# Performance work log

Hardware: AMD Instinct MI355X
Metric: run time of the kernel (lower is better)

## Reference

```python
import jax, jax.numpy as jnp
import numpy as np

N_NODES = 20000
N_EDGES = 640000
HIDDEN = 256
MSG = 64  # discrete message of MSG binary symbols -> 2*MSG one-hot bits
TAU = 0.5


def setup_inputs() -> dict:
    key = jax.random.key(0)
    ks = jax.random.split(key, 12)
    x = jax.random.normal(ks[0], (N_NODES, HIDDEN), dtype=jnp.float32)
    h = jax.random.normal(ks[1], (N_NODES, HIDDEN), dtype=jnp.float32)
    src = jax.random.randint(ks[2], (N_EDGES,), 0, N_NODES)
    dst = jax.random.randint(ks[3], (N_EDGES,), 0, N_NODES)
    u = jax.random.uniform(ks[4], (N_EDGES, MSG, 2), dtype=jnp.float32,
                           minval=1e-6, maxval=1.0 - 1e-6)
    gumbel = -jnp.log(-jnp.log(u))  # standard Gumbel noise
    def lin(k, out_f, in_f):
        bound = 1.0 / np.sqrt(in_f)
        kw, kb = jax.random.split(k)
        W = jax.random.uniform(kw, (out_f, in_f), jnp.float32, -bound, bound)
        b = jax.random.uniform(kb, (out_f,), jnp.float32, -bound, bound)
        return W, b
    W_enc, b_enc = lin(ks[5], 2 * MSG, 2 * HIDDEN)          # f_enc
    W_dec, b_dec = lin(ks[6], 2 * MSG, 2 * MSG)             # f_dec
    W_ih, b_ih = lin(ks[7], 3 * HIDDEN, HIDDEN + 2 * MSG)   # GRUCell input weights
    W_hh, b_hh = lin(ks[8], 3 * HIDDEN, HIDDEN)             # GRUCell hidden weights
    return dict(x=x, h=h, W_enc=W_enc, b_enc=b_enc, W_dec=W_dec, b_dec=b_dec,
                W_ih=W_ih, b_ih=b_ih, W_hh=W_hh, b_hh=b_hh,
                gumbel=gumbel, src=src, dst=dst)


def reference(x, h, W_enc, b_enc, W_dec, b_dec, W_ih, b_ih, W_hh, b_hh,
              gumbel, src, dst):
    N = x.shape[0]
    h_det = jax.lax.stop_gradient(h)  # edges.src['h'] uses h.detach()
    # --- msg_func: per-edge encode + straight-through gumbel-softmax (hard) ---
    e_in = jnp.concatenate([x[src], h_det[src]], axis=1)           # [E, 2H]
    logits = (e_in @ W_enc.T + b_enc).reshape(-1, MSG, 2)          # [E, M, 2]
    y_soft = jax.nn.softmax((logits + gumbel) / TAU, axis=-1)
    y_hard = jax.nn.one_hot(jnp.argmax(y_soft, axis=-1), 2, dtype=y_soft.dtype)
    m = (y_hard + y_soft - jax.lax.stop_gradient(y_soft)).reshape(-1, 2 * MSG)
    # --- aggr_func: elementwise-OR == segment max over destination nodes ---
    c = jax.ops.segment_max(m, dst, num_segments=N)
    c = jnp.where(jnp.isneginf(c), 0.0, c)  # nodes with no in-edges get zeros
    # --- update: f_dec + GRUCell (PyTorch gate order r, z, n) ---
    inp = jnp.concatenate([x, c @ W_dec.T + b_dec], axis=1)        # [N, H+2M]
    gi = inp @ W_ih.T + b_ih                                       # [N, 3H]
    gh = h @ W_hh.T + b_hh                                         # [N, 3H]
    i_r, i_z, i_n = jnp.split(gi, 3, axis=1)
    h_r, h_z, h_n = jnp.split(gh, 3, axis=1)
    r = jax.nn.sigmoid(i_r + h_r)
    z = jax.nn.sigmoid(i_z + h_z)
    n = jnp.tanh(i_n + r * h_n)
    return (1.0 - z) * n + z * h
```

## Files before the change

kernel.cpp:

```cpp
#include <hip/hip_runtime.h>
#include <math.h>

#define NN 20000
#define NE 640000

typedef __attribute__((ext_vector_type(8))) short short8v;
typedef __attribute__((ext_vector_type(4))) float f32x4;

__device__ inline unsigned short f2bf(float f) {
    unsigned int u = __builtin_bit_cast(unsigned int, f);
    u += 0x7fff + ((u >> 16) & 1);
    return (unsigned short)(u >> 16);
}
__device__ inline float bf2f(unsigned short s) {
    unsigned int u = ((unsigned int)s) << 16;
    return __builtin_bit_cast(float, u);
}
__device__ inline void gload16(const unsigned short* g, short* l) {
    __builtin_amdgcn_global_load_lds(
        (const __attribute__((address_space(1))) unsigned int*)g,
        (__attribute__((address_space(3))) unsigned int*)l, 16, 0, 0);
}

__global__ __launch_bounds__(512)
void enc_prep(const float* __restrict__ x, const float* __restrict__ h,
              const float* __restrict__ W_enc, const float* __restrict__ b_enc,
              const float* __restrict__ W_ih, const float* __restrict__ W_hh,
              const float* __restrict__ W_dec, const float* __restrict__ b_ih,
              const float* __restrict__ b_hh, const float* __restrict__ b_dec,
              unsigned short* __restrict__ LdiffBf, unsigned short* __restrict__ Abig,
              unsigned short* __restrict__ Wbig, float* __restrict__ bias_cat,
              unsigned int* __restrict__ cbits)
{
    const int tid = threadIdx.x;
    if (blockIdx.x >= 313) {
        const int r = blockIdx.x - 313;
        int zi = r * 512 + tid;
        if (zi < NN * 4) cbits[zi] = 0u;
        const int g = r >> 8, j = r & 255;
        {
            float v;
            if (tid < 256) {
                v = (g < 3) ? W_ih[(size_t)(g * 256 + j) * 384 + tid] : 0.f;
            } else {
                int sr = (g < 2) ? g * 256 + j : 512 + j;
                v = (g == 2) ? 0.f : W_hh[(size_t)sr * 256 + (tid - 256)];
            }
            Wbig[(size_t)r * 640 + tid] = f2bf(v);
        }
        if (tid < 128) {
            float acc = 0.f;
            if (g < 3) {
                const float* wr = W_ih + (size_t)(g * 256 + j) * 384 + 256;
#pragma unroll 4
                for (int p = 0; p < 128; ++p) acc += wr[p] * W_dec[p * 128 + tid];
            }
            Wbig[(size_t)r * 640 + 512 + tid] = f2bf(acc);
        } else if (tid < 192) {
            int m = tid - 128;
            float v = 0.f;
            if (g < 3) {
                const float* wr = W_ih + (size_t)(g * 256 + j) * 384 + 256;
                v = wr[m] * b_dec[m] + wr[m + 64] * b_dec[m + 64];
            }
#pragma unroll
            for (int o = 1; o < 64; o <<= 1) v += __shfl_xor(v, o);
            if (m == 0) {
                float bv;
                if (g == 3) bv = b_hh[512 + j];
                else {
                    int sr = g * 256 + j;
                    bv = b_ih[sr] + v + ((g < 2) ? b_hh[sr] : 0.f);
                }
                bias_cat[r] = bv;
            }
        }
        return;
    }
    __shared__ __align__(16) short Ah[64][72], Al[64][72];
    __shared__ __align__(16) short Wh[128 * 64], Wl[128 * 64];
    const int bm0 = blockIdx.x * 64;
    const int lane = tid & 63;
    const int wave = tid >> 6;
    const int wm = wave >> 2, wn = wave & 3;
    const int r16 = lane & 15, kg = lane >> 4;
    const int sw = r16 & 7;

    const int arow = tid >> 3, as_ = tid & 7;
    const int agm = (bm0 + arow >= NN) ? NN - 1 : bm0 + arow;
    const int wrow0 = tid >> 3, wrow1 = (tid >> 3) + 64, ws_ = tid & 7;

    f32x4 acc[2][2];
#pragma unroll
    for (int i = 0; i < 2; ++i)
#pragma unroll
        for (int j = 0; j < 2; ++j) acc[i][j] = (f32x4){0.f, 0.f, 0.f, 0.f};

    float4 av0, av1, wv0, wv1, wv2, wv3;
    auto ISSUE = [&](int kt) {
        int kc = kt * 64 + as_ * 8;
        const float* p = (kc < 256) ? (x + (size_t)agm * 256 + kc)
                                    : (h + (size_t)agm * 256 + (kc - 256));
        av0 = *(const float4*)p;
        av1 = *(const float4*)(p + 4);
        const float* q0 = W_enc + (size_t)wrow0 * 512 + kt * 64 + ws_ * 8;
        const float* q1 = W_enc + (size_t)wrow1 * 512 + kt * 64 + ws_ * 8;
        wv0 = *(const float4*)q0; wv1 = *(const float4*)(q0 + 4);
        wv2 = *(const float4*)q1; wv3 = *(const float4*)(q1 + 4);
    };

    ISSUE(0);
    for (int kt = 0; kt < 8; ++kt) {
        __syncthreads();
        {
            float vv[8] = {av0.x, av0.y, av0.z, av0.w, av1.x, av1.y, av1.z, av1.w};
            short8v hi, lo;
#pragma unroll
            for (int t = 0; t < 8; ++t) {
                unsigned short hb = f2bf(vv[t]);
                hi[t] = (short)hb;
                lo[t] = (short)f2bf(vv[t] - bf2f(hb));
            }
            *(short8v*)&Ah[arow][as_ * 8] = hi;
            *(short8v*)&Al[arow][as_ * 8] = lo;
            __builtin_nontemporal_store(
                hi, (short8v*)&Abig[(size_t)agm * 512 + kt * 64 + as_ * 8]);
            float ww0[8] = {wv0.x, wv0.y, wv0.z, wv0.w, wv1.x, wv1.y, wv1.z, wv1.w};
            float ww1[8] = {wv2.x, wv2.y, wv2.z, wv2.w, wv3.x, wv3.y, wv3.z, wv3.w};
            short8v h0, l0, h1, l1;
#pragma unroll
            for (int t = 0; t < 8; ++t) {
                unsigned short hb0 = f2bf(ww0[t]);
                h0[t] = (short)hb0; l0[t] = (short)f2bf(ww0[t] - bf2f(hb0));
                unsigned short hb1 = f2bf(ww1[t]);
                h1[t] = (short)hb1; l1[t] = (short)f2bf(ww1[t] - bf2f(hb1));
            }
            int p0 = (ws_ ^ (wrow0 & 7)) * 8;
            int p1 = (ws_ ^ (wrow1 & 7)) * 8;
            *(short8v*)&Wh[wrow0 * 64 + p0] = h0;
            *(short8v*)&Wl[wrow0 * 64 + p0] = l0;
            *(short8v*)&Wh[wrow1 * 64 + p1] = h1;
            *(short8v*)&Wl[wrow1 * 64 + p1] = l1;
        }
        if (kt < 7) ISSUE(kt + 1);
        __syncthreads();
#pragma unroll
        for (int ks = 0; ks < 2; ++ks) {
            int kc = ks * 32 + kg * 8;
            int gsel = (ks * 4 + kg) ^ sw;
            short8v ah[2], al[2], wh[2], wl[2];
#pragma unroll
            for (int f = 0; f < 2; ++f) {
                ah[f] = *(const short8v*)&Ah[wm * 32 + f * 16 + r16][kc];
                al[f] = *(const short8v*)&Al[wm * 32 + f * 16 + r16][kc];
                int wr = wn * 32 + f * 16 + r16;
                wh[f] = *(const short8v*)&Wh[wr * 64 + gsel * 8];
                wl[f] = *(const short8v*)&Wl[wr * 64 + gsel * 8];
            }
#pragma unroll
            for (int fi = 0; fi < 2; ++fi)
#pragma unroll
                for (int fj = 0; fj < 2; ++fj) {
                    acc[fi][fj] = __builtin_amdgcn_mfma_f32_16x16x32_bf16(
                        ah[fi], wh[fj], acc[fi][fj], 0, 0, 0);
                    acc[fi][fj] = __builtin_amdgcn_mfma_f32_16x16x32_bf16(
                        al[fi], wh[fj], acc[fi][fj], 0, 0, 0);
                    acc[fi][fj] = __builtin_amdgcn_mfma_f32_16x16x32_bf16(
                        ah[fi], wl[fj], acc[fi][fj], 0, 0, 0);
                }
        }
    }
#pragma unroll
    for (int fi = 0; fi < 2; ++fi) {
        int rg = bm0 + wm * 32 + fi * 16 + kg * 4;
#pragma unroll
        for (int fj = 0; fj < 2; ++fj) {
            int cg = wn * 32 + fj * 16 + r16;
            float bv = b_enc[cg];
#pragma unroll
            for (int i = 0; i < 4; ++i) {
                float v = acc[fi][fj][i] + bv;
                float o = __shfl_xor(v, 1);
                if (!(r16 & 1) && rg + i < NN)
                    LdiffBf[(size_t)(rg + i) * 64 + (cg >> 1)] = f2bf(v - o);
            }
        }
    }
}

__global__ __launch_bounds__(256)
void edge_msg_kernel(const unsigned short* __restrict__ LdiffBf,
                     const float* __restrict__ gumbel,
                     const int* __restrict__ src, const int* __restrict__ dst,
                     unsigned long long* __restrict__ cbits64, int E)
{
    const int lane = threadIdx.x & 63;
    const int hl = lane & 31;
    const int side = lane >> 5;
    const int slot = blockIdx.x * 4 + (threadIdx.x >> 6);
    const int nslots = gridDim.x * 4;
    const unsigned int* Lw = (const unsigned int*)LdiffBf;

    int p0 = slot;
    if (p0 * 2 >= E) return;
    int e0 = p0 * 2 + side;
    int s0 = src[e0], d0n = dst[e0];
    f32x4 g0 = __builtin_nontemporal_load(
        (const f32x4*)&gumbel[(size_t)e0 * 128 + hl * 4]);
    unsigned int L0 = Lw[(size_t)s0 * 32 + hl];
    int p1 = p0 + nslots;
    int s1 = 0, d1n = 0;
    if (p1 * 2 < E) { int e1 = p1 * 2 + side; s1 = src[e1]; d1n = dst[e1]; }

    while (true) {
        const bool more1 = p1 * 2 < E;
        f32x4 g1; unsigned int L1 = 0;
        if (more1) {
            int e1 = p1 * 2 + side;
            g1 = __builtin_nontemporal_load(
                (const f32x4*)&gumbel[(size_t)e1 * 128 + hl * 4]);
            L1 = Lw[(size_t)s1 * 32 + hl];
        }
        int p2 = p1 + nslots;
        int s2 = 0, d2n = 0;
        if (p2 * 2 < E) { int e2 = p2 * 2 + side; s2 = src[e2]; d2n = dst[e2]; }
        float da = bf2f((unsigned short)(L0 & 0xffffu));
        float db = bf2f((unsigned short)(L0 >> 16));
        int c0 = (da + g0[0]) < g0[1] ? 1 : 0;
        int c1 = (db + g0[2]) < g0[3] ? 1 : 0;
        int sh = (hl & 7) * 4;
        unsigned int val = (1u << (sh + c0)) | (1u << (sh + 2 + c1));
        val |= __shfl_xor(val, 1);
        val |= __shfl_xor(val, 2);
        val |= __shfl_xor(val, 4);
        unsigned int hiw = __shfl_xor(val, 8);
        if ((hl & 15) == 0)
            atomicOr(&cbits64[(size_t)d0n * 2 + (hl >> 4)],
                     (unsigned long long)val | ((unsigned long long)hiw << 32));
        if (!more1) break;
        p0 = p1; s0 = s1; d0n = d1n; g0 = g1; L0 = L1;
        p1 = p2; s1 = s2; d1n = d2n;
    }
}

__global__ __launch_bounds__(256)
void gates_gru(const unsigned short* __restrict__ Abig,
               const unsigned int* __restrict__ cbits,
               const unsigned short* __restrict__ Wbig,
               const float* __restrict__ bias_cat,
               const float* __restrict__ h, float* __restrict__ out)
{
    __shared__ __align__(16) short As[2][64 * 64];
    const int orig = blockIdx.x;
    const int xcd = orig & 7, idx = orig >> 3;
    const int wgid = (xcd < 4 ? xcd * 157 : 628 + (xcd - 4) * 156) + idx;
    const int bm0 = (wgid >> 2) * 64;
    const int j0  = (wgid & 3) * 64;
    const int tid = threadIdx.x;
    const int lane = tid & 63;
    const int w = tid >> 6;
    const int r16 = lane & 15, kg = lane >> 4;
    const int sw = r16 & 7;

    f32x4 acc[4][4];
#pragma unroll
    for (int g = 0; g < 4; ++g)
#pragma unroll
        for (int i = 0; i < 4; ++i) acc[g][i] = (f32x4){0.f, 0.f, 0.f, 0.f};

    unsigned int cw[4][4];
#pragma unroll
    for (int fi = 0; fi < 4; ++fi) {
        int rr = bm0 + fi * 16 + r16; if (rr >= NN) rr = NN - 1;
        uint4 v = *(const uint4*)&cbits[rr * 4];
        cw[fi][0] = v.x; cw[fi][1] = v.y; cw[fi][2] = v.z; cw[fi][3] = v.w;
    }

    auto STAGE = [&](int b, int kt) {
        const int kc0 = kt * 64;
#pragma unroll
        for (int it = 0; it < 2; ++it) {
            int chunk = w * 2 + it;
            int slot = chunk * 64 + lane;
            int row = slot >> 3, gch = slot & 7;
            int gm = bm0 + row; if (gm >= NN) gm = NN - 1;
            gload16(Abig + (size_t)gm * 512 + kc0 + ((gch ^ (row & 7)) << 3),
                    As[b] + chunk * 512);
        }
    };
    short8v breg[2][3][2];
    auto BLOAD = [&](int b, int kt) {
        const int kc0 = kt * 64;
        const int g2 = (kt < 4 || kt >= 8) ? 2 : 3;
#pragma unroll
        for (int s = 0; s < 3; ++s) {
            int gate = (s < 2) ? s : g2;
            const unsigned short* bp =
                Wbig + (size_t)(gate * 256 + j0 + w * 16 + r16) * 640 + kc0 + kg * 8;
            breg[b][s][0] = *(const short8v*)bp;
            breg[b][s][1] = *(const short8v*)(bp + 32);
        }
    };

    STAGE(0, 0);
    BLOAD(0, 0);
#pragma unroll
    for (int kt = 0; kt < 8; ++kt) {
        const int cur = kt & 1;
        if (kt < 7) STAGE(cur ^ 1, kt + 1);
        BLOAD(cur ^ 1, kt + 1);
        if (kt < 7) { asm volatile("s_waitcnt vmcnt(8)" ::: "memory"); }
        else        { asm volatile("s_waitcnt vmcnt(6)" ::: "memory"); }
        __builtin_amdgcn_s_barrier();
        __builtin_amdgcn_sched_barrier(0);
        const int g2c = (kt < 4) ? 2 : 3;
        __builtin_amdgcn_s_setprio(1);
#pragma unroll
        for (int ks = 0; ks < 2; ++ks) {
            int gsel = (ks * 4 + kg) ^ sw;
            short8v a[4];
#pragma unroll
            for (int fi = 0; fi < 4; ++fi)
                a[fi] = *(const short8v*)&As[cur][(fi * 16 + r16) * 64 + gsel * 8];
#pragma unroll
            for (int s = 0; s < 3; ++s) {
                const int gate = (s < 2) ? s : g2c;
#pragma unroll
                for (int fi = 0; fi < 4; ++fi)
                    acc[gate][fi] = __builtin_amdgcn_mfma_f32_16x16x32_bf16(
                        a[fi], breg[cur][s][ks], acc[gate][fi], 0, 0, 0);
            }
        }
        __builtin_amdgcn_s_setprio(0);
        __builtin_amdgcn_sched_barrier(0);
        __builtin_amdgcn_s_barrier();
    }
    BLOAD(1, 9);
#pragma unroll
    for (int kt8 = 0; kt8 < 2; ++kt8) {
        short8v a[4][2];
#pragma unroll
        for (int fi = 0; fi < 4; ++fi)
#pragma unroll
            for (int ks = 0; ks < 2; ++ks) {
                unsigned int byte = (cw[fi][kt8 * 2 + ks] >> (kg * 8)) & 0xffu;
                short8v v;
#pragma unroll
                for (int t = 0; t < 8; ++t)
                    v[t] = ((byte >> t) & 1u) ? (short)0x3F80 : (short)0;
                a[fi][ks] = v;
            }
#pragma unroll
        for (int ks = 0; ks < 2; ++ks)
#pragma unroll
            for (int s = 0; s < 3; ++s) {
                const int gate = (s < 2) ? s : 2;
#pragma unroll
                for (int fi = 0; fi < 4; ++fi)
                    acc[gate][fi] = __builtin_amdgcn_mfma_f32_16x16x32_bf16(
                        a[fi][ks], breg[kt8][s][ks], acc[gate][fi], 0, 0, 0);
            }
    }
    const int cg = j0 + w * 16 + r16;
    const float br = bias_cat[cg],       bz = bias_cat[256 + cg];
    const float bi = bias_cat[512 + cg], bh = bias_cat[768 + cg];
#pragma unroll
    for (int fi = 0; fi < 4; ++fi) {
        int rg = bm0 + fi * 16 + kg * 4;
#pragma unroll
        for (int i = 0; i < 4; ++i) {
            int m = rg + i;
            if (m >= NN) continue;
            float rp = acc[0][fi][i] + br;
            float zp = acc[1][fi][i] + bz;
            float ip = acc[2][fi][i] + bi;
            float hp = acc[3][fi][i] + bh;
            float hv = h[(size_t)m * 256 + cg];
            float r = 1.f / (1.f + __expf(-rp));
            float z = 1.f / (1.f + __expf(-zp));
            float nn2 = tanhf(ip + r * hp);
            __builtin_nontemporal_store((1.f - z) * nn2 + z * hv,
                                        &out[(size_t)m * 256 + cg]);
        }
    }
}

extern "C" void kernel_launch(void* const* d_in, const int* in_sizes, int n_in,
                              void* d_out, int out_size, void* d_ws, size_t ws_size,
                              hipStream_t stream)
{
    const float* x     = (const float*)d_in[0];
    const float* h     = (const float*)d_in[1];
    const float* W_enc = (const float*)d_in[2];
    const float* b_enc = (const float*)d_in[3];
    const float* W_dec = (const float*)d_in[4];
    const float* b_dec = (const float*)d_in[5];
    const float* W_ih  = (const float*)d_in[6];
    const float* b_ih  = (const float*)d_in[7];
    const float* W_hh  = (const float*)d_in[8];
    const float* b_hh  = (const float*)d_in[9];
    const float* gumbel = (const float*)d_in[10];
    const int*   src   = (const int*)d_in[11];
    const int*   dst   = (const int*)d_in[12];
    float* out = (float*)d_out;

    char* ws = (char*)d_ws;
    unsigned short* LdiffBf  = (unsigned short*)(ws);
    unsigned int*   cbits    = (unsigned int*)(ws + 2560000);
    unsigned short* Wbig     = (unsigned short*)(ws + 2880000);
    float*          bias_cat = (float*)(ws + 4190720);
    unsigned short* Abig     = (unsigned short*)(ws + 4194816);

    enc_prep<<<1337, 512, 0, stream>>>(x, h, W_enc, b_enc, W_ih, W_hh, W_dec,
                                       b_ih, b_hh, b_dec,
                                       LdiffBf, Abig, Wbig, bias_cat, cbits);
    edge_msg_kernel<<<4096, 256, 0, stream>>>(LdiffBf, gumbel, src, dst,
                                              (unsigned long long*)cbits, NE);
    gates_gru<<<1252, 256, 0, stream>>>(Abig, cbits, Wbig, bias_cat, h, out);
}
```

Baseline: 156.1 us.

## Overlap edge messaging with x/h gate GEMM and split c-dependent tail

Merges the edge message/atomic-OR pass and the x/h part of the GRU gate GEMM into one launch, with block index choosing the role. The goal is to let the memory-bound edge scatter run at the same time as the MFMA-heavy GEMM. Because the GEMM no longer waits for the aggregated bits, its partial accumulators go to a bf16 preactivation buffer. A new tail kernel reloads them, adds the c·W contribution from the bit-packed messages, and applies the GRU nonlinearity. The cost is an extra round trip of preactivations through global memory and bf16 rounding of those partial sums, which may reduce accuracy. It also drops the nontemporal hint on the Abig store, likely to keep the data cache-resident.

```diff
diff --git a/kernel.cpp b/kernel.cpp
--- a/kernel.cpp
+++ b/kernel.cpp
@@ -123,8 +123,7 @@
             }
             *(short8v*)&Ah[arow][as_ * 8] = hi;
             *(short8v*)&Al[arow][as_ * 8] = lo;
-            __builtin_nontemporal_store(
-                hi, (short8v*)&Abig[(size_t)agm * 512 + kt * 64 + as_ * 8]);
+            *(short8v*)&Abig[(size_t)agm * 512 + kt * 64 + as_ * 8] = hi;
             float ww0[8] = {wv0.x, wv0.y, wv0.z, wv0.w, wv1.x, wv1.y, wv1.z, wv1.w};
             float ww1[8] = {wv2.x, wv2.y, wv2.z, wv2.w, wv3.x, wv3.y, wv3.z, wv3.w};
             short8v h0, l0, h1, l1;
@@ -189,74 +188,71 @@
 }
 
 __global__ __launch_bounds__(256)
-void edge_msg_kernel(const unsigned short* __restrict__ LdiffBf,
-                     const float* __restrict__ gumbel,
-                     const int* __restrict__ src, const int* __restrict__ dst,
-                     unsigned long long* __restrict__ cbits64, int E)
+void edge_gatesxh(const unsigned short* __restrict__ LdiffBf,
+                  const float* __restrict__ gumbel,
+                  const int* __restrict__ src, const int* __restrict__ dst,
+                  unsigned long long* __restrict__ cbits64,
+                  const unsigned short* __restrict__ Abig,
+                  const unsigned short* __restrict__ Wbig,
+                  unsigned short* __restrict__ preact, int E)
 {
-    const int lane = threadIdx.x & 63;
-    const int hl = lane & 31;
-    const int side = lane >> 5;
-    const int slot = blockIdx.x * 4 + (threadIdx.x >> 6);
-    const int nslots = gridDim.x * 4;
-    const unsigned int* Lw = (const unsigned int*)LdiffBf;
-
-    int p0 = slot;
-    if (p0 * 2 >= E) return;
-    int e0 = p0 * 2 + side;
-    int s0 = src[e0], d0n = dst[e0];
-    f32x4 g0 = __builtin_nontemporal_load(
-        (const f32x4*)&gumbel[(size_t)e0 * 128 + hl * 4]);
-    unsigned int L0 = Lw[(size_t)s0 * 32 + hl];
-    int p1 = p0 + nslots;
-    int s1 = 0, d1n = 0;
-    if (p1 * 2 < E) { int e1 = p1 * 2 + side; s1 = src[e1]; d1n = dst[e1]; }
-
-    while (true) {
-        const bool more1 = p1 * 2 < E;
-        f32x4 g1; unsigned int L1 = 0;
-        if (more1) {
-            int e1 = p1 * 2 + side;
-            g1 = __builtin_nontemporal_load(
-                (const f32x4*)&gumbel[(size_t)e1 * 128 + hl * 4]);
-            L1 = Lw[(size_t)s1 * 32 + hl];
-        }
-        int p2 = p1 + nslots;
-        int s2 = 0, d2n = 0;
-        if (p2 * 2 < E) { int e2 = p2 * 2 + side; s2 = src[e2]; d2n = dst[e2]; }
-        float da = bf2f((unsigned short)(L0 & 0xffffu));
-        float db = bf2f((unsigned short)(L0 >> 16));
-        int c0 = (da + g0[0]) < g0[1] ? 1 : 0;
-        int c1 = (db + g0[2]) < g0[3] ? 1 : 0;
-        int sh = (hl & 7) * 4;
-        unsigned int val = (1u << (sh + c0)) | (1u << (sh + 2 + c1));
-        val |= __shfl_xor(val, 1);
-        val |= __shfl_xor(val, 2);
-        val |= __shfl_xor(val, 4);
-        unsigned int hiw = __shfl_xor(val, 8);
-        if ((hl & 15) == 0)
-            atomicOr(&cbits64[(size_t)d0n * 2 + (hl >> 4)],
-                     (unsigned long long)val | ((unsigned long long)hiw << 32));
-        if (!more1) break;
-        p0 = p1; s0 = s1; d0n = d1n; g0 = g1; L0 = L1;
-        p1 = p2; s1 = s2; d1n = d2n;
-    }
-}
-
-__global__ __launch_bounds__(256)
-void gates_gru(const unsigned short* __restrict__ Abig,
-               const unsigned int* __restrict__ cbits,
-               const unsigned short* __restrict__ Wbig,
-               const float* __restrict__ bias_cat,
-               const float* __restrict__ h, float* __restrict__ out)
-{
+    const int tid = threadIdx.x;
+    if (blockIdx.x < 2048) {
+        const int lane = tid & 63;
+        const int hl = lane & 31;
+        const int side = lane >> 5;
+        const int slot = blockIdx.x * 4 + (tid >> 6);
+        const int nslots = 2048 * 4;
+        const unsigned int* Lw = (const unsigned int*)LdiffBf;
+
+        int p0 = slot;
+        if (p0 * 2 >= E) return;
+        int e0 = p0 * 2 + side;
+        int s0 = src[e0], d0n = dst[e0];
+        f32x4 g0 = __builtin_nontemporal_load(
+            (const f32x4*)&gumbel[(size_t)e0 * 128 + hl * 4]);
+        unsigned int L0 = Lw[(size_t)s0 * 32 + hl];
+        int p1 = p0 + nslots;
+        int s1 = 0, d1n = 0;
+        if (p1 * 2 < E) { int e1 = p1 * 2 + side; s1 = src[e1]; d1n = dst[e1]; }
+
+        while (true) {
+            const bool more1 = p1 * 2 < E;
+            f32x4 g1; unsigned int L1 = 0;
+            if (more1) {
+                int e1 = p1 * 2 + side;
+                g1 = __builtin_nontemporal_load(
+                    (const f32x4*)&gumbel[(size_t)e1 * 128 + hl * 4]);
+                L1 = Lw[(size_t)s1 * 32 + hl];
+            }
+            int p2 = p1 + nslots;
+            int s2 = 0, d2n = 0;
+            if (p2 * 2 < E) { int e2 = p2 * 2 + side; s2 = src[e2]; d2n = dst[e2]; }
+            float da = bf2f((unsigned short)(L0 & 0xffffu));
+            float db = bf2f((unsigned short)(L0 >> 16));
+            int c0 = (da + g0[0]) < g0[1] ? 1 : 0;
+            int c1 = (db + g0[2]) < g0[3] ? 1 : 0;
+            int sh = (hl & 7) * 4;
+            unsigned int val = (1u << (sh + c0)) | (1u << (sh + 2 + c1));
+            val |= __shfl_xor(val, 1);
+            val |= __shfl_xor(val, 2);
+            val |= __shfl_xor(val, 4);
+            unsigned int hiw = __shfl_xor(val, 8);
+            if ((hl & 15) == 0)
+                atomicOr(&cbits64[(size_t)d0n * 2 + (hl >> 4)],
+                         (unsigned long long)val | ((unsigned long long)hiw << 32));
+            if (!more1) break;
+            p0 = p1; s0 = s1; d0n = d1n; g0 = g1; L0 = L1;
+            p1 = p2; s1 = s2; d1n = d2n;
+        }
+        return;
+    }
     __shared__ __align__(16) short As[2][64 * 64];
-    const int orig = blockIdx.x;
+    const int orig = blockIdx.x - 2048;
     const int xcd = orig & 7, idx = orig >> 3;
     const int wgid = (xcd < 4 ? xcd * 157 : 628 + (xcd - 4) * 156) + idx;
     const int bm0 = (wgid >> 2) * 64;
     const int j0  = (wgid & 3) * 64;
-    const int tid = threadIdx.x;
     const int lane = tid & 63;
     const int w = tid >> 6;
     const int r16 = lane & 15, kg = lane >> 4;
@@ -267,14 +263,6 @@
     for (int g = 0; g < 4; ++g)
 #pragma unroll
         for (int i = 0; i < 4; ++i) acc[g][i] = (f32x4){0.f, 0.f, 0.f, 0.f};
-
-    unsigned int cw[4][4];
-#pragma unroll
-    for (int fi = 0; fi < 4; ++fi) {
-        int rr = bm0 + fi * 16 + r16; if (rr >= NN) rr = NN - 1;
-        uint4 v = *(const uint4*)&cbits[rr * 4];
-        cw[fi][0] = v.x; cw[fi][1] = v.y; cw[fi][2] = v.z; cw[fi][3] = v.w;
-    }
 
     auto STAGE = [&](int b, int kt) {
         const int kc0 = kt * 64;
@@ -291,7 +279,7 @@
     short8v breg[2][3][2];
     auto BLOAD = [&](int b, int kt) {
         const int kc0 = kt * 64;
-        const int g2 = (kt < 4 || kt >= 8) ? 2 : 3;
+        const int g2 = (kt < 4) ? 2 : 3;
 #pragma unroll
         for (int s = 0; s < 3; ++s) {
             int gate = (s < 2) ? s : g2;
@@ -307,10 +295,13 @@
 #pragma unroll
     for (int kt = 0; kt < 8; ++kt) {
         const int cur = kt & 1;
-        if (kt < 7) STAGE(cur ^ 1, kt + 1);
-        BLOAD(cur ^ 1, kt + 1);
-        if (kt < 7) { asm volatile("s_waitcnt vmcnt(8)" ::: "memory"); }
-        else        { asm volatile("s_waitcnt vmcnt(6)" ::: "memory"); }
+        if (kt < 7) {
+            STAGE(cur ^ 1, kt + 1);
+            BLOAD(cur ^ 1, kt + 1);
+            asm volatile("s_waitcnt vmcnt(8)" ::: "memory");
+        } else {
+            asm volatile("s_waitcnt vmcnt(0)" ::: "memory");
+        }
         __builtin_amdgcn_s_barrier();
         __builtin_amdgcn_sched_barrier(0);
         const int g2c = (kt < 4) ? 2 : 3;
@@ -335,7 +326,68 @@
         __builtin_amdgcn_sched_barrier(0);
         __builtin_amdgcn_s_barrier();
     }
-    BLOAD(1, 9);
+    const int cg = j0 + w * 16 + r16;
+#pragma unroll
+    for (int g = 0; g < 4; ++g)
+#pragma unroll
+        for (int fi = 0; fi < 4; ++fi) {
+            int rg = bm0 + fi * 16 + kg * 4;
+#pragma unroll
+            for (int i = 0; i < 4; ++i) {
+                int m = rg + i;
+                if (m < NN)
+                    __builtin_nontemporal_store(
+                        f2bf(acc[g][fi][i]),
+                        &preact[(size_t)m * 1024 + g * 256 + cg]);
+            }
+        }
+}
+
+__global__ __launch_bounds__(256)
+void gru_ctail(const unsigned short* __restrict__ preact,
+               const unsigned int* __restrict__ cbits,
+               const unsigned short* __restrict__ Wbig,
+               const float* __restrict__ bias_cat,
+               const float* __restrict__ h, float* __restrict__ out)
+{
+    const int wgid = blockIdx.x;
+    const int bm0 = (wgid >> 2) * 64;
+    const int j0  = (wgid & 3) * 64;
+    const int tid = threadIdx.x;
+    const int lane = tid & 63;
+    const int w = tid >> 6;
+    const int r16 = lane & 15, kg = lane >> 4;
+    const int cg = j0 + w * 16 + r16;
+
+    unsigned int cw[4][4];
+#pragma unroll
+    for (int fi = 0; fi < 4; ++fi) {
+        int rr = bm0 + fi * 16 + r16; if (rr >= NN) rr = NN - 1;
+        uint4 v = *(const uint4*)&cbits[rr * 4];
+        cw[fi][0] = v.x; cw[fi][1] = v.y; cw[fi][2] = v.z; cw[fi][3] = v.w;
+    }
+    short8v breg[2][3][2];
+#pragma unroll
+    for (int kt8 = 0; kt8 < 2; ++kt8)
+#pragma unroll
+        for (int s = 0; s < 3; ++s) {
+            const unsigned short* bp =
+                Wbig + (size_t)(s * 256 + j0 + w * 16 + r16) * 640 + (8 + kt8) * 64 + kg * 8;
+            breg[kt8][s][0] = *(const short8v*)bp;
+            breg[kt8][s][1] = *(const short8v*)(bp + 32);
+        }
+    f32x4 acc[4][4];
+#pragma unroll
+    for (int g = 0; g < 4; ++g)
+#pragma unroll
+        for (int fi = 0; fi < 4; ++fi) {
+            int rg = bm0 + fi * 16 + kg * 4;
+#pragma unroll
+            for (int i = 0; i < 4; ++i) {
+                int m = rg + i; if (m >= NN) m = NN - 1;
+                acc[g][fi][i] = bf2f(preact[(size_t)m * 1024 + g * 256 + cg]);
+            }
+        }
 #pragma unroll
     for (int kt8 = 0; kt8 < 2; ++kt8) {
         short8v a[4][2];
@@ -361,7 +413,6 @@
                         a[fi][ks], breg[kt8][s][ks], acc[gate][fi], 0, 0, 0);
             }
     }
-    const int cg = j0 + w * 16 + r16;
     const float br = bias_cat[cg],       bz = bias_cat[256 + cg];
     const float bi = bias_cat[512 + cg], bh = bias_cat[768 + cg];
 #pragma unroll
@@ -410,11 +461,13 @@
     unsigned short* Wbig     = (unsigned short*)(ws + 2880000);
     float*          bias_cat = (float*)(ws + 4190720);
     unsigned short* Abig     = (unsigned short*)(ws + 4194816);
+    unsigned short* preact   = (unsigned short*)(ws + 24674816);
 
     enc_prep<<<1337, 512, 0, stream>>>(x, h, W_enc, b_enc, W_ih, W_hh, W_dec,
                                        b_ih, b_hh, b_dec,
                                        LdiffBf, Abig, Wbig, bias_cat, cbits);
-    edge_msg_kernel<<<4096, 256, 0, stream>>>(LdiffBf, gumbel, src, dst,
-                                              (unsigned long long*)cbits, NE);
-    gates_gru<<<1252, 256, 0, stream>>>(Abig, cbits, Wbig, bias_cat, h, out);
-}
+    edge_gatesxh<<<3300, 256, 0, stream>>>(LdiffBf, gumbel, src, dst,
+                                           (unsigned long long*)cbits,
+                                           Abig, Wbig, preact, NE);
+    gru_ctail<<<1252, 256, 0, stream>>>(preact, cbits, Wbig, bias_cat, h, out);
+}
```

New measurement: 199.9 us. +28.1%, slower.
